# Performance work log

Measured on AMD Instinct MI355X. Metric: run time of the kernel, lower is better.

## Reference

```python
import jax, jax.numpy as jnp
import numpy as np

B, T = 256, 512          # sequences, timesteps (batched over pyro.markov loop)
DATA_DIM = 88            # piano-roll tones
HIDDEN_DIM = 16          # HMM latent states
NN_DIM = 48
NN_CHANNELS = 2
KERNEL = 3


def _uniform(key, shape, fan_in):
    bound = 1.0 / np.sqrt(fan_in)
    return jax.random.uniform(key, shape, minval=-bound, maxval=bound, dtype=jnp.float32)


def setup_inputs() -> dict:
    key = jax.random.key(0)
    ks = jax.random.split(key, 13)
    w = jax.random.randint(ks[0], (B, T, 1), 0, HIDDEN_DIM)
    x = jax.random.randint(ks[1], (B, T, 1), 0, HIDDEN_DIM)
    y = jax.random.uniform(ks[2], (B, T, DATA_DIM), dtype=jnp.float32)
    return {
        "w": w, "x": x, "y": y,
        # nn.Linear(hidden_dim, nn_dim) for x and w one-hots
        "W_xh": _uniform(ks[3], (NN_DIM, HIDDEN_DIM), HIDDEN_DIM),
        "b_xh": _uniform(ks[4], (NN_DIM,), HIDDEN_DIM),
        "W_wh": _uniform(ks[5], (NN_DIM, HIDDEN_DIM), HIDDEN_DIM),
        "b_wh": _uniform(ks[6], (NN_DIM,), HIDDEN_DIM),
        # nn.Linear(nn_channels*data_dim, nn_dim)
        "W_yh": _uniform(ks[7], (NN_DIM, NN_CHANNELS * DATA_DIM), NN_CHANNELS * DATA_DIM),
        "b_yh": _uniform(ks[8], (NN_DIM,), NN_CHANNELS * DATA_DIM),
        # nn.Conv1d(1, nn_channels, 3, padding=1)
        "W_conv": _uniform(ks[9], (NN_CHANNELS, 1, KERNEL), KERNEL),
        "b_conv": _uniform(ks[10], (NN_CHANNELS,), KERNEL),
        # nn.Linear(nn_dim, data_dim)
        "W_hl": _uniform(ks[11], (DATA_DIM, NN_DIM), NN_DIM),
        "b_hl": _uniform(ks[12], (DATA_DIM,), NN_DIM),
    }


def _tones_generator(w, x, y, W_xh, b_xh, W_wh, b_wh, W_yh, b_yh, W_conv, b_conv, W_hl, b_hl):
    b, t, d = y.shape
    # one-hot scatter of the latent state indices (trailing index dim of size 1)
    w_onehot = jax.nn.one_hot(w[..., 0], HIDDEN_DIM, dtype=y.dtype)   # [B,T,H]
    x_onehot = jax.nn.one_hot(x[..., 0], HIDDEN_DIM, dtype=y.dtype)   # [B,T,H]
    # Conv1d(1 -> nn_channels, k=3, pad=1) over the tone axis
    y_nch = y.reshape(b * t, 1, d)                                    # [BT,1,D]
    y_conv = jax.lax.conv_general_dilated(
        y_nch, W_conv, window_strides=(1,), padding=[(1, 1)],
        dimension_numbers=("NCH", "OIH", "NCH"))
    y_conv = jax.nn.relu(y_conv + b_conv[None, :, None])              # [BT,C,D]
    y_conv = y_conv.reshape(b, t, NN_CHANNELS * d)                    # [B,T,C*D]
    h = jax.nn.relu(
        jnp.einsum("bth,nh->btn", x_onehot, W_xh) + b_xh
        + jnp.einsum("bth,nh->btn", w_onehot, W_wh) + b_wh
        + jnp.einsum("btc,nc->btn", y_conv, W_yh) + b_yh)             # [B,T,ND]
    return jnp.einsum("btn,dn->btd", h, W_hl) + b_hl                  # [B,T,D]


def reference(w, x, y, W_xh, b_xh, W_wh, b_wh, W_yh, b_yh, W_conv, b_conv, W_hl, b_hl):
    return _tones_generator(w, x, y, W_xh, b_xh, W_wh, b_wh, W_yh, b_yh,
                            W_conv, b_conv, W_hl, b_hl)
```

## Files before the change

kernel.cpp:

```cpp
#include <hip/hip_runtime.h>
#include <stdint.h>

#define NTOK (256 * 512)
#define TPB 256

typedef short bf16x8 __attribute__((ext_vector_type(8)));
typedef float f32x4 __attribute__((ext_vector_type(4)));
typedef unsigned short u16;
typedef unsigned int u32;

#define B1_U16 10752
#define B2_U16 6144

__device__ __forceinline__ u16 f2bf(float f) {
    u32 u = __float_as_uint(f);
    return (u16)((u + 0x7fffu + ((u >> 16) & 1u)) >> 16);
}

__global__ __launch_bounds__(256, 1)
void prep_weights(const float* __restrict__ Wxh, const float* __restrict__ bxh,
                  const float* __restrict__ Wwh, const float* __restrict__ bwh,
                  const float* __restrict__ Wyh, const float* __restrict__ byh,
                  const float* __restrict__ Whl, const float* __restrict__ bhl,
                  u16* __restrict__ ws)
{
    int e = blockIdx.x * 256 + threadIdx.x;
    if (e < B1_U16) {
        int j = e & 7, n = (e >> 3) % 48, kc = e / 384;
        int k = kc * 8 + j;
        float v;
        if (k < 176)       v = Wyh[n * 176 + (k & 1) * 88 + (k >> 1)];
        else if (k < 192)  v = Wxh[n * 16 + (k - 176)];
        else if (k < 208)  v = Wwh[n * 16 + (k - 192)];
        else if (k == 208) v = bxh[n] + bwh[n] + byh[n];
        else               v = 0.0f;
        ws[e] = f2bf(v);
    } else if (e < B1_U16 + B2_U16) {
        int e2 = e - B1_U16;
        int j = e2 & 7, dd = (e2 >> 3) % 96, kc = e2 / 768;
        int k = kc * 8 + j;
        float v = 0.0f;
        if (dd < 88) {
            if (k < 48)       v = Whl[dd * 48 + k];
            else if (k == 48) v = bhl[dd];
        }
        ws[e] = f2bf(v);
    }
}

struct Tile { float4 v[6]; int xv, wv; };

__global__ __launch_bounds__(256, 2)
void tones_v6(const int* __restrict__ widx, const int* __restrict__ xidx,
              const float* __restrict__ y,
              const float* __restrict__ Wconv, const float* __restrict__ bconv,
              const u16* __restrict__ wsb,
              float* __restrict__ out)
{
    __shared__ __align__(16) u16 sB2[B2_U16];
    __shared__ __align__(16) u16 sH[4 * 1024];

    const int tid = threadIdx.x;
    const int wave = tid >> 6, lane = tid & 63;
    const int q = lane >> 4, c = lane & 15;

    {
        const uint4* src = (const uint4*)(wsb + B1_U16);
        uint4* dst = (uint4*)sB2;
        #pragma unroll
        for (int i = 0; i < 3; i++) dst[tid + 256 * i] = src[tid + 256 * i];
    }

    bf16x8 B1[7][3];
    #pragma unroll
    for (int ks = 0; ks < 7; ks++)
        #pragma unroll
        for (int nt = 0; nt < 3; nt++)
            B1[ks][nt] = *(const bf16x8*)(wsb + ((ks * 4 + q) * 48 + nt * 16 + c) * 8);

    const float wc00 = Wconv[0], wc01 = Wconv[1], wc02 = Wconv[2];
    const float wc10 = Wconv[3], wc11 = Wconv[4], wc12 = Wconv[5];
    const float bc0 = bconv[0], bc1 = bconv[1];
    __syncthreads();

    u16* sW = sH + wave * 1024;
    if (lane < 32) {
        uint4 hz = make_uint4((lane < 16) ? 0x3F80u : 0u, 0, 0, 0);
        *(uint4*)(sW + ((6 + (lane >> 4)) * 16 + (lane & 15)) * 8) = hz;
    }

    const int base = blockIdx.x * 256 + wave * 64;

    auto load_tile = [&](int t, Tile& T) {
        const int tb = base + t * 16;
        const float* yc = y + (size_t)(tb + c) * 88;
        #pragma unroll
        for (int s = 0; s < 5; s++)
            T.v[s] = *(const float4*)(yc + 16 * s + 4 * q);
        if (q < 2) T.v[5] = *(const float4*)(yc + 80 + 4 * q);
        else       T.v[5] = make_float4(0.f, 0.f, 0.f, 0.f);
        T.xv = xidx[tb + c];
        T.wv = widx[tb + c];
    };

    auto compute_tile = [&](int t, const Tile& T) {
        const int tb = base + t * 16;
        const float* yc = y + (size_t)(tb + c) * 88;
        f32x4 h0 = {0, 0, 0, 0}, h1 = {0, 0, 0, 0}, h2 = {0, 0, 0, 0};

        #pragma unroll
        for (int s = 0; s < 5; s++) {
            const int d0 = 16 * s + 4 * q;
            float p0 = (d0 == 0) ? 0.0f : yc[d0 - 1];
            float p5 = yc[d0 + 4];
            float p[6] = {p0, T.v[s].x, T.v[s].y, T.v[s].z, T.v[s].w, p5};
            bf16x8 af;
            #pragma unroll
            for (int i = 0; i < 4; i++) {
                float c0 = fmaf(wc00, p[i], fmaf(wc01, p[i + 1], fmaf(wc02, p[i + 2], bc0)));
                float c1 = fmaf(wc10, p[i], fmaf(wc11, p[i + 1], fmaf(wc12, p[i + 2], bc1)));
                af[2 * i]     = (short)f2bf(fmaxf(c0, 0.0f));
                af[2 * i + 1] = (short)f2bf(fmaxf(c1, 0.0f));
            }
            h0 = __builtin_amdgcn_mfma_f32_16x16x32_bf16(af, B1[s][0], h0, 0, 0, 0);
            h1 = __builtin_amdgcn_mfma_f32_16x16x32_bf16(af, B1[s][1], h1, 0, 0, 0);
            h2 = __builtin_amdgcn_mfma_f32_16x16x32_bf16(af, B1[s][2], h2, 0, 0, 0);
        }
        {
            bf16x8 af;
            if (q < 2) {
                const int d0 = 80 + 4 * q;
                float p0 = yc[d0 - 1];
                float p5 = (q == 0) ? yc[84] : 0.0f;
                float p[6] = {p0, T.v[5].x, T.v[5].y, T.v[5].z, T.v[5].w, p5};
                #pragma unroll
                for (int i = 0; i < 4; i++) {
                    float c0 = fmaf(wc00, p[i], fmaf(wc01, p[i + 1], fmaf(wc02, p[i + 2], bc0)));
                    float c1 = fmaf(wc10, p[i], fmaf(wc11, p[i + 1], fmaf(wc12, p[i + 2], bc1)));
                    af[2 * i]     = (short)f2bf(fmaxf(c0, 0.0f));
                    af[2 * i + 1] = (short)f2bf(fmaxf(c1, 0.0f));
                }
            } else {
                const int bse = (q - 2) * 8;
                #pragma unroll
                for (int j = 0; j < 8; j++)
                    af[j] = (short)((bse + j == T.xv) ? 0x3F80 : 0);
            }
            h0 = __builtin_amdgcn_mfma_f32_16x16x32_bf16(af, B1[5][0], h0, 0, 0, 0);
            h1 = __builtin_amdgcn_mfma_f32_16x16x32_bf16(af, B1[5][1], h1, 0, 0, 0);
            h2 = __builtin_amdgcn_mfma_f32_16x16x32_bf16(af, B1[5][2], h2, 0, 0, 0);
        }
        {
            bf16x8 af;
            if (q < 2) {
                const int bse = q * 8;
                #pragma unroll
                for (int j = 0; j < 8; j++)
                    af[j] = (short)((bse + j == T.wv) ? 0x3F80 : 0);
            } else {
                #pragma unroll
                for (int j = 0; j < 8; j++)
                    af[j] = (short)((q == 2 && j == 0) ? 0x3F80 : 0);
            }
            h0 = __builtin_amdgcn_mfma_f32_16x16x32_bf16(af, B1[6][0], h0, 0, 0, 0);
            h1 = __builtin_amdgcn_mfma_f32_16x16x32_bf16(af, B1[6][1], h1, 0, 0, 0);
            h2 = __builtin_amdgcn_mfma_f32_16x16x32_bf16(af, B1[6][2], h2, 0, 0, 0);
        }

        #pragma unroll
        for (int r = 0; r < 4; r++) {
            const int row = q * 4 + r;
            sW[((0 + (c >> 3)) * 16 + row) * 8 + (c & 7)] = f2bf(fmaxf(h0[r], 0.0f));
            sW[((2 + (c >> 3)) * 16 + row) * 8 + (c & 7)] = f2bf(fmaxf(h1[r], 0.0f));
            sW[((4 + (c >> 3)) * 16 + row) * 8 + (c & 7)] = f2bf(fmaxf(h2[r], 0.0f));
        }

        f32x4 o0 = {0,0,0,0}, o1 = {0,0,0,0}, o2 = {0,0,0,0};
        f32x4 o3 = {0,0,0,0}, o4 = {0,0,0,0}, o5 = {0,0,0,0};
        #pragma unroll
        for (int ks = 0; ks < 2; ks++) {
            bf16x8 a2 = *(const bf16x8*)(sW + ((ks * 4 + q) * 16 + c) * 8);
            bf16x8 b;
            b = *(const bf16x8*)(sB2 + ((ks * 4 + q) * 96 +  0 + c) * 8);
            o0 = __builtin_amdgcn_mfma_f32_16x16x32_bf16(a2, b, o0, 0, 0, 0);
            b = *(const bf16x8*)(sB2 + ((ks * 4 + q) * 96 + 16 + c) * 8);
            o1 = __builtin_amdgcn_mfma_f32_16x16x32_bf16(a2, b, o1, 0, 0, 0);
            b = *(const bf16x8*)(sB2 + ((ks * 4 + q) * 96 + 32 + c) * 8);
            o2 = __builtin_amdgcn_mfma_f32_16x16x32_bf16(a2, b, o2, 0, 0, 0);
            b = *(const bf16x8*)(sB2 + ((ks * 4 + q) * 96 + 48 + c) * 8);
            o3 = __builtin_amdgcn_mfma_f32_16x16x32_bf16(a2, b, o3, 0, 0, 0);
            b = *(const bf16x8*)(sB2 + ((ks * 4 + q) * 96 + 64 + c) * 8);
            o4 = __builtin_amdgcn_mfma_f32_16x16x32_bf16(a2, b, o4, 0, 0, 0);
            b = *(const bf16x8*)(sB2 + ((ks * 4 + q) * 96 + 80 + c) * 8);
            o5 = __builtin_amdgcn_mfma_f32_16x16x32_bf16(a2, b, o5, 0, 0, 0);
        }

        float* orow = out + (size_t)(tb + q * 4) * 88;
        #pragma unroll
        for (int r = 0; r < 4; r++) {
            orow[r * 88 +  0 + c] = o0[r];
            orow[r * 88 + 16 + c] = o1[r];
            orow[r * 88 + 32 + c] = o2[r];
            orow[r * 88 + 48 + c] = o3[r];
            orow[r * 88 + 64 + c] = o4[r];
            if (c < 8) orow[r * 88 + 80 + c] = o5[r];
        }
    };

    Tile TA, TB;
    load_tile(0, TA);
    load_tile(1, TB);  compute_tile(0, TA);
    load_tile(2, TA);  compute_tile(1, TB);
    load_tile(3, TB);  compute_tile(2, TA);
    compute_tile(3, TB);
}

extern "C" void kernel_launch(void* const* d_in, const int* in_sizes, int n_in,
                              void* d_out, int out_size, void* d_ws, size_t ws_size,
                              hipStream_t stream) {
    (void)in_sizes; (void)n_in; (void)out_size; (void)ws_size;
    u16* ws = (u16*)d_ws;
    prep_weights<<<dim3(66), dim3(TPB), 0, stream>>>(
        (const float*)d_in[3],  (const float*)d_in[4],
        (const float*)d_in[5],  (const float*)d_in[6],
        (const float*)d_in[7],  (const float*)d_in[8],
        (const float*)d_in[11], (const float*)d_in[12], ws);
    tones_v6<<<dim3(NTOK / 256), dim3(TPB), 0, stream>>>(
        (const int*)d_in[0], (const int*)d_in[1], (const float*)d_in[2],
        (const float*)d_in[9], (const float*)d_in[10], ws, (float*)d_out);
}
```

Baseline: 137.0 us.

## Raise occupancy: move sparse weight slices to LDS, shuffle conv halos, halve tiles

The fused conv+MLP kernel now keeps only the five dense B1 k-slices in registers. The two one-hot/bias slices move to shared memory, and launch bounds go from 2 to 4 blocks per CU. Conv halo neighbours now come from wave shuffles instead of extra global loads. Each block handles 128 tokens (2 tiles per wave, no software double-buffering), and the grid is doubled. The aim is to cut register pressure and redundant loads so more waves hide latency, at the cost of losing explicit load/compute overlap and repeating the weight-staging prologue across twice as many blocks.

```diff
diff --git a/kernel.cpp b/kernel.cpp
--- a/kernel.cpp
+++ b/kernel.cpp
@@ -11,6 +11,8 @@
 
 #define B1_U16 10752
 #define B2_U16 6144
+#define B1T_OFF 7680
+#define B1T_U16 3072
 
 __device__ __forceinline__ u16 f2bf(float f) {
     u32 u = __float_as_uint(f);
@@ -48,16 +50,15 @@
     }
 }
 
-struct Tile { float4 v[6]; int xv, wv; };
-
-__global__ __launch_bounds__(256, 2)
-void tones_v6(const int* __restrict__ widx, const int* __restrict__ xidx,
+__global__ __launch_bounds__(256, 4)
+void tones_v7(const int* __restrict__ widx, const int* __restrict__ xidx,
               const float* __restrict__ y,
               const float* __restrict__ Wconv, const float* __restrict__ bconv,
               const u16* __restrict__ wsb,
               float* __restrict__ out)
 {
     __shared__ __align__(16) u16 sB2[B2_U16];
+    __shared__ __align__(16) u16 sB1t[B1T_U16];
     __shared__ __align__(16) u16 sH[4 * 1024];
 
     const int tid = threadIdx.x;
@@ -65,15 +66,17 @@
     const int q = lane >> 4, c = lane & 15;
 
     {
-        const uint4* src = (const uint4*)(wsb + B1_U16);
-        uint4* dst = (uint4*)sB2;
-        #pragma unroll
-        for (int i = 0; i < 3; i++) dst[tid + 256 * i] = src[tid + 256 * i];
-    }
-
-    bf16x8 B1[7][3];
+        const uint4* s2 = (const uint4*)(wsb + B1_U16);
+        uint4* d2 = (uint4*)sB2;
+        d2[tid] = s2[tid]; d2[tid + 256] = s2[tid + 256]; d2[tid + 512] = s2[tid + 512];
+        const uint4* s1 = (const uint4*)(wsb + B1T_OFF);
+        uint4* d1 = (uint4*)sB1t;
+        d1[tid] = s1[tid];
+        if (tid < 128) d1[256 + tid] = s1[256 + tid];
+    }
+    bf16x8 B1[5][3];
     #pragma unroll
-    for (int ks = 0; ks < 7; ks++)
+    for (int ks = 0; ks < 5; ks++)
         #pragma unroll
         for (int nt = 0; nt < 3; nt++)
             B1[ks][nt] = *(const bf16x8*)(wsb + ((ks * 4 + q) * 48 + nt * 16 + c) * 8);
@@ -89,31 +92,30 @@
         *(uint4*)(sW + ((6 + (lane >> 4)) * 16 + (lane & 15)) * 8) = hz;
     }
 
-    const int base = blockIdx.x * 256 + wave * 64;
-
-    auto load_tile = [&](int t, Tile& T) {
+    const int base = blockIdx.x * 128 + wave * 32;
+    const int lup = (lane + 16) & 63, ldn = (lane + 48) & 63;
+
+    #pragma unroll 1
+    for (int t = 0; t < 2; t++) {
         const int tb = base + t * 16;
         const float* yc = y + (size_t)(tb + c) * 88;
-        #pragma unroll
-        for (int s = 0; s < 5; s++)
-            T.v[s] = *(const float4*)(yc + 16 * s + 4 * q);
-        if (q < 2) T.v[5] = *(const float4*)(yc + 80 + 4 * q);
-        else       T.v[5] = make_float4(0.f, 0.f, 0.f, 0.f);
-        T.xv = xidx[tb + c];
-        T.wv = widx[tb + c];
-    };
-
-    auto compute_tile = [&](int t, const Tile& T) {
-        const int tb = base + t * 16;
-        const float* yc = y + (size_t)(tb + c) * 88;
+        float4 v[6];
+        #pragma unroll
+        for (int s = 0; s < 5; s++) v[s] = *(const float4*)(yc + 16 * s + 4 * q);
+        v[5] = (q < 2) ? *(const float4*)(yc + 80 + 4 * q) : make_float4(0.f, 0.f, 0.f, 0.f);
+        const int xv = xidx[tb + c];
+        const int wv = widx[tb + c];
+
         f32x4 h0 = {0, 0, 0, 0}, h1 = {0, 0, 0, 0}, h2 = {0, 0, 0, 0};
 
         #pragma unroll
         for (int s = 0; s < 5; s++) {
-            const int d0 = 16 * s + 4 * q;
-            float p0 = (d0 == 0) ? 0.0f : yc[d0 - 1];
-            float p5 = yc[d0 + 4];
-            float p[6] = {p0, T.v[s].x, T.v[s].y, T.v[s].z, T.v[s].w, p5};
+            float send1 = (q == 0) ? v[s + 1].x : v[s].x;
+            float p5 = __shfl(send1, lup);
+            float send0 = (q == 3) ? ((s > 0) ? v[s - 1].w : v[0].w) : v[s].w;
+            float p0 = __shfl(send0, ldn);
+            if (s == 0 && q == 0) p0 = 0.0f;
+            float p[6] = {p0, v[s].x, v[s].y, v[s].z, v[s].w, p5};
             bf16x8 af;
             #pragma unroll
             for (int i = 0; i < 4; i++) {
@@ -127,12 +129,13 @@
             h2 = __builtin_amdgcn_mfma_f32_16x16x32_bf16(af, B1[s][2], h2, 0, 0, 0);
         }
         {
+            float p5 = __shfl(v[5].x, lup);
+            float send0 = (q == 3) ? v[4].w : v[5].w;
+            float p0 = __shfl(send0, ldn);
             bf16x8 af;
             if (q < 2) {
-                const int d0 = 80 + 4 * q;
-                float p0 = yc[d0 - 1];
-                float p5 = (q == 0) ? yc[84] : 0.0f;
-                float p[6] = {p0, T.v[5].x, T.v[5].y, T.v[5].z, T.v[5].w, p5};
+                if (q == 1) p5 = 0.0f;
+                float p[6] = {p0, v[5].x, v[5].y, v[5].z, v[5].w, p5};
                 #pragma unroll
                 for (int i = 0; i < 4; i++) {
                     float c0 = fmaf(wc00, p[i], fmaf(wc01, p[i + 1], fmaf(wc02, p[i + 2], bc0)));
@@ -144,11 +147,14 @@
                 const int bse = (q - 2) * 8;
                 #pragma unroll
                 for (int j = 0; j < 8; j++)
-                    af[j] = (short)((bse + j == T.xv) ? 0x3F80 : 0);
+                    af[j] = (short)((bse + j == xv) ? 0x3F80 : 0);
             }
-            h0 = __builtin_amdgcn_mfma_f32_16x16x32_bf16(af, B1[5][0], h0, 0, 0, 0);
-            h1 = __builtin_amdgcn_mfma_f32_16x16x32_bf16(af, B1[5][1], h1, 0, 0, 0);
-            h2 = __builtin_amdgcn_mfma_f32_16x16x32_bf16(af, B1[5][2], h2, 0, 0, 0);
+            bf16x8 b0 = *(const bf16x8*)(sB1t + ((0 * 4 + q) * 48 +  0 + c) * 8);
+            bf16x8 b1 = *(const bf16x8*)(sB1t + ((0 * 4 + q) * 48 + 16 + c) * 8);
+            bf16x8 b2 = *(const bf16x8*)(sB1t + ((0 * 4 + q) * 48 + 32 + c) * 8);
+            h0 = __builtin_amdgcn_mfma_f32_16x16x32_bf16(af, b0, h0, 0, 0, 0);
+            h1 = __builtin_amdgcn_mfma_f32_16x16x32_bf16(af, b1, h1, 0, 0, 0);
+            h2 = __builtin_amdgcn_mfma_f32_16x16x32_bf16(af, b2, h2, 0, 0, 0);
         }
         {
             bf16x8 af;
@@ -156,15 +162,18 @@
                 const int bse = q * 8;
                 #pragma unroll
                 for (int j = 0; j < 8; j++)
-                    af[j] = (short)((bse + j == T.wv) ? 0x3F80 : 0);
+                    af[j] = (short)((bse + j == wv) ? 0x3F80 : 0);
             } else {
                 #pragma unroll
                 for (int j = 0; j < 8; j++)
                     af[j] = (short)((q == 2 && j == 0) ? 0x3F80 : 0);
             }
-            h0 = __builtin_amdgcn_mfma_f32_16x16x32_bf16(af, B1[6][0], h0, 0, 0, 0);
-            h1 = __builtin_amdgcn_mfma_f32_16x16x32_bf16(af, B1[6][1], h1, 0, 0, 0);
-            h2 = __builtin_amdgcn_mfma_f32_16x16x32_bf16(af, B1[6][2], h2, 0, 0, 0);
+            bf16x8 b0 = *(const bf16x8*)(sB1t + ((1 * 4 + q) * 48 +  0 + c) * 8);
+            bf16x8 b1 = *(const bf16x8*)(sB1t + ((1 * 4 + q) * 48 + 16 + c) * 8);
+            bf16x8 b2 = *(const bf16x8*)(sB1t + ((1 * 4 + q) * 48 + 32 + c) * 8);
+            h0 = __builtin_amdgcn_mfma_f32_16x16x32_bf16(af, b0, h0, 0, 0, 0);
+            h1 = __builtin_amdgcn_mfma_f32_16x16x32_bf16(af, b1, h1, 0, 0, 0);
+            h2 = __builtin_amdgcn_mfma_f32_16x16x32_bf16(af, b2, h2, 0, 0, 0);
         }
 
         #pragma unroll
@@ -205,14 +214,7 @@
             orow[r * 88 + 64 + c] = o4[r];
             if (c < 8) orow[r * 88 + 80 + c] = o5[r];
         }
-    };
-
-    Tile TA, TB;
-    load_tile(0, TA);
-    load_tile(1, TB);  compute_tile(0, TA);
-    load_tile(2, TA);  compute_tile(1, TB);
-    load_tile(3, TB);  compute_tile(2, TA);
-    compute_tile(3, TB);
+    }
 }
 
 extern "C" void kernel_launch(void* const* d_in, const int* in_sizes, int n_in,
@@ -225,7 +227,7 @@
         (const float*)d_in[5],  (const float*)d_in[6],
         (const float*)d_in[7],  (const float*)d_in[8],
         (const float*)d_in[11], (const float*)d_in[12], ws);
-    tones_v6<<<dim3(NTOK / 256), dim3(TPB), 0, stream>>>(
+    tones_v7<<<dim3(NTOK / 128), dim3(TPB), 0, stream>>>(
         (const int*)d_in[0], (const int*)d_in[1], (const float*)d_in[2],
         (const float*)d_in[9], (const float*)d_in[10], ws, (float*)d_out);
 }
```

New measurement: 164.4 us. +20.0%, slower.
